# Kernel optimization log

Measured on AMD Instinct MI355X. Metric: run time of the kernel, lower is better.

## Reference

```python
import jax, jax.numpy as jnp
import numpy as np

NONLIN = jnp.tanh  # configurable gate/candidate nonlinearity ('nonlin' init arg)

T, B, I, H = 1024, 64, 256, 512


def setup_inputs() -> dict:
    key = jax.random.key(0)
    k1, k2, k3 = jax.random.split(key, 3)
    s_i = 1.0 / np.sqrt(I)
    s_h = 1.0 / np.sqrt(H)
    return {
        "x": jax.random.normal(k1, (T, B, I), dtype=jnp.float32),
        "Wi": jax.random.normal(k2, (I, 4 * H), dtype=jnp.float32) * s_i,
        "Wh": jax.random.normal(k3, (H, 4 * H), dtype=jnp.float32) * s_h,
        "bi": jnp.zeros((4 * H,), dtype=jnp.float32),
        "bh": jnp.zeros((4 * H,), dtype=jnp.float32),
        "h0": jnp.zeros((B, H), dtype=jnp.float32),
        "c0": jnp.zeros((B, H), dtype=jnp.float32),
    }


def reference(x, Wi, Wh, bi, bh, h0, c0):
    # Precompute input projection for all timesteps in one big GEMM: [T,B,4H]
    x_proj = jnp.einsum('tbi,ig->tbg', x, Wi) + bi

    def step(carry, xp_t):
        h, c = carry
        gates = xp_t + h @ Wh + bh            # [B, 4H]
        i_g, f_g, g_g, o_g = jnp.split(gates, 4, axis=-1)
        i_g = jax.nn.sigmoid(i_g)
        f_g = jax.nn.sigmoid(f_g)
        o_g = jax.nn.sigmoid(o_g)
        g_g = NONLIN(g_g)
        c_new = f_g * c + i_g * g_g
        h_new = o_g * NONLIN(c_new)
        return (h_new, c_new), h_new

    (h_T, c_T), hs = jax.lax.scan(step, (h0, c0), x_proj)
    return hs  # [T, B, H] hidden states for every timestep
```

## Files before the change

kernel.cpp:

```cpp
#include <hip/hip_runtime.h>
#include <math.h>


#define TT      1024
#define BB      64
#define II      256
#define HH      512
#define G4H     2048
#define RPB     16
#define NRG     4
#define NCG     64
#define THREADS 512

typedef short  bf16x8 __attribute__((ext_vector_type(8)));
typedef float  f32x4  __attribute__((ext_vector_type(4)));

__device__ __forceinline__ unsigned int cvtpk_bf16(float a, float b) {
    unsigned int r;
    asm volatile("v_cvt_pk_bf16_f32 %0, %1, %2" : "=v"(r) : "v"(a), "v"(b));
    return r;
}

__device__ __forceinline__ void coh_load4_f4(const float* p0, const float* p1,
                                             const float* p2, const float* p3,
                                             float4& a, float4& b,
                                             float4& c, float4& d) {
    asm volatile(
        "global_load_dwordx4 %0, %4, off sc0 sc1\n\t"
        "global_load_dwordx4 %1, %5, off sc0 sc1\n\t"
        "global_load_dwordx4 %2, %6, off sc0 sc1\n\t"
        "global_load_dwordx4 %3, %7, off sc0 sc1\n\t"
        "s_waitcnt vmcnt(0)"
        : "=&v"(a), "=&v"(b), "=&v"(c), "=&v"(d)
        : "v"(p0), "v"(p1), "v"(p2), "v"(p3)
        : "memory");
}
__device__ __forceinline__ void coh_store_f(float* p, float v) {
    asm volatile("global_store_dword %0, %1, off sc0 sc1"
                 :: "v"(p), "v"(v) : "memory");
}
__device__ __forceinline__ float fast_tanh(float v) {
    const float e = __expf(-2.0f * fabsf(v));
    const float r = (1.0f - e) / (1.0f + e);
    return v < 0.0f ? -r : r;
}
__device__ __forceinline__ float sigm(float v) {
    return 1.0f / (1.0f + __expf(-v));
}

__device__ __forceinline__ void stage_a(bf16x8* FH, bf16x8* FL,
                                        int kk, int r, int sub, float4 v) {
    const int lane_s = r + 16 * (sub >> 3);
    const int ui     = (sub & 7) >> 1;
    const unsigned int h0 = cvtpk_bf16(v.x, v.y);
    const unsigned int h1 = cvtpk_bf16(v.z, v.w);
    const float ax = __uint_as_float(h0 << 16);
    const float ay = __uint_as_float(h0 & 0xffff0000u);
    const float az = __uint_as_float(h1 << 16);
    const float aw = __uint_as_float(h1 & 0xffff0000u);
    const unsigned int l0 = cvtpk_bf16(v.x - ax, v.y - ay);
    const unsigned int l1 = cvtpk_bf16(v.z - az, v.w - aw);
    unsigned int* ph = (unsigned int*)&FH[kk * 64 + lane_s];
    unsigned int* pl = (unsigned int*)&FL[kk * 64 + lane_s];
    ph[ui] = h0; ph[ui + 1] = h1;
    pl[ui] = l0; pl[ui + 1] = l1;
}

__global__ void init_ctr(unsigned int* ctr) { ctr[threadIdx.x] = 0; }

__global__ __launch_bounds__(THREADS) void lstm_persist(
    const float* __restrict__ x,
    const float* __restrict__ Wi,
    const float* __restrict__ Wh,
    const float* __restrict__ bi,
    const float* __restrict__ bh,
    const float* __restrict__ h0p,
    const float* __restrict__ c0p,
    float* __restrict__ out,
    unsigned int* __restrict__ ctr)
{
    const int tid   = threadIdx.x;
    const int cg    = blockIdx.x & 63;
    const int rg    = blockIdx.x >> 6;
    const int row0  = rg * RPB;
    const int cell0 = cg * 8;
    const int wv    = tid >> 6;
    const int lane  = tid & 63;
    const int n2    = wv >> 2;
    const int k4    = wv & 3;

    __shared__ bf16x8 aFH[24 * 64];
    __shared__ bf16x8 aFL[24 * 64];
    __shared__ bf16x8 bFH[48 * 64];
    __shared__ bf16x8 bFL[48 * 64];
    __shared__ float  red[8 * 64 * 4];
    __shared__ float  c_lds[RPB][8];

    for (int i = 0; i < 24; ++i) {
        const int u     = tid + THREADS * i;
        const int upos  = u & 3;
        const int slice = u >> 2;
        const int lane_ = slice & 63;
        const int kk    = (slice >> 6) % 24;
        const int nn    = (slice >> 6) / 24;
        const int e0    = upos * 2;
        const int k     = kk * 32 + (lane_ >> 4) * 8 + e0;
        const int col   = nn * 16 + (lane_ & 15);
        const int J     = (col >> 3) * HH + cell0 + (col & 7);
        const float w0  = (k < II) ? Wi[(size_t)k * G4H + J]
                                   : Wh[(size_t)(k - II) * G4H + J];
        const float w1  = (k < II) ? Wi[(size_t)(k + 1) * G4H + J]
                                   : Wh[(size_t)(k + 1 - II) * G4H + J];
        const unsigned int hi = cvtpk_bf16(w0, w1);
        const float f0 = __uint_as_float(hi << 16);
        const float f1 = __uint_as_float(hi & 0xffff0000u);
        const unsigned int lo = cvtpk_bf16(w0 - f0, w1 - f1);
        ((unsigned int*)bFH)[u] = hi;
        ((unsigned int*)bFL)[u] = lo;
    }

    float b4[4];
    if (tid < 128) {
        const int r = tid >> 3, m8 = tid & 7;
        #pragma unroll
        for (int g = 0; g < 4; ++g)
            b4[g] = bi[g * HH + cell0 + m8] + bh[g * HH + cell0 + m8];
        c_lds[r][m8] = c0p[(size_t)(row0 + r) * HH + cell0 + m8];
    }

    #pragma unroll
    for (int i = 0; i < 2; ++i) {
        const int s = tid + THREADS * i, r = s >> 6, k = 4 * (s & 63);
        const float4 v = *(const float4*)(x + (size_t)(row0 + r) * II + k);
        stage_a(aFH, aFL, k >> 5, r, k & 31, v);
    }
    #pragma unroll
    for (int i = 0; i < 4; ++i) {
        const int s = tid + THREADS * i, r = s >> 7, k = 4 * (s & 127);
        const float4 v = *(const float4*)(h0p + (size_t)(row0 + r) * HH + k);
        stage_a(aFH, aFL, 8 + (k >> 5), r, k & 31, v);
    }
    __syncthreads();

    f32x4 acc = {0.f, 0.f, 0.f, 0.f};
    #pragma unroll
    for (int q = 0; q < 2; ++q) {
        const int kk = k4 * 2 + q;
        const bf16x8 ah = aFH[kk * 64 + lane];
        const bf16x8 al = aFL[kk * 64 + lane];
        const bf16x8 wh = bFH[(n2 * 24 + kk) * 64 + lane];
        const bf16x8 wl = bFL[(n2 * 24 + kk) * 64 + lane];
        acc = __builtin_amdgcn_mfma_f32_16x16x32_bf16(ah, wh, acc, 0, 0, 0);
        acc = __builtin_amdgcn_mfma_f32_16x16x32_bf16(ah, wl, acc, 0, 0, 0);
        acc = __builtin_amdgcn_mfma_f32_16x16x32_bf16(al, wh, acc, 0, 0, 0);
    }

    unsigned int* myctr = ctr + rg * 32;

    for (int t = 0; t < TT; ++t) {
        const bool more = (t + 1 < TT);

        float4 xr0, xr1;
        int xk0, xr0r, xk1, xr1r;
        if (more) {
            const int s0 = tid;       xr0r = s0 >> 6; xk0 = 4 * (s0 & 63);
            const int s1 = tid + 512; xr1r = s1 >> 6; xk1 = 4 * (s1 & 63);
            xr0 = *(const float4*)(x + ((size_t)(t + 1) * BB + row0 + xr0r) * II + xk0);
            xr1 = *(const float4*)(x + ((size_t)(t + 1) * BB + row0 + xr1r) * II + xk1);
        }

        #pragma unroll
        for (int q = 0; q < 4; ++q) {
            const int kk = 8 + k4 * 4 + q;
            const bf16x8 ah = aFH[kk * 64 + lane];
            const bf16x8 al = aFL[kk * 64 + lane];
            const bf16x8 wh = bFH[(n2 * 24 + kk) * 64 + lane];
            const bf16x8 wl = bFL[(n2 * 24 + kk) * 64 + lane];
            acc = __builtin_amdgcn_mfma_f32_16x16x32_bf16(ah, wh, acc, 0, 0, 0);
            acc = __builtin_amdgcn_mfma_f32_16x16x32_bf16(ah, wl, acc, 0, 0, 0);
            acc = __builtin_amdgcn_mfma_f32_16x16x32_bf16(al, wh, acc, 0, 0, 0);
        }

        ((f32x4*)red)[wv * 64 + lane] = acc;
        if (more) {
            stage_a(aFH, aFL, xk0 >> 5, xr0r, xk0 & 31, xr0);
            stage_a(aFH, aFL, xk1 >> 5, xr1r, xk1 & 31, xr1);
        }
        __syncthreads();

        if (tid < 128) {
            const int r = tid >> 3, m8 = tid & 7;
            const int lane_c_base = 16 * (r >> 2);
            const int reg = r & 3;
            float g4[4];
            #pragma unroll
            for (int g = 0; g < 4; ++g) {
                const int col = g * 8 + m8;
                const int nn  = col >> 4, cl = col & 15;
                const int lc  = cl + lane_c_base;
                float s = b4[g];
                #pragma unroll
                for (int p = 0; p < 4; ++p)
                    s += red[((nn * 4 + p) * 64 + lc) * 4 + reg];
                g4[g] = s;
            }
            const float ig = sigm(g4[0]);
            const float fg = sigm(g4[1]);
            const float gg = fast_tanh(g4[2]);
            const float og = sigm(g4[3]);
            const float cn = fg * c_lds[r][m8] + ig * gg;
            c_lds[r][m8] = cn;
            coh_store_f(out + ((size_t)t * BB + row0 + r) * HH + cell0 + m8,
                        og * fast_tanh(cn));
        }

        asm volatile("s_waitcnt vmcnt(0) lgkmcnt(0)" ::: "memory");
        __syncthreads();
        if (more) {
            if (tid == 0)
                __hip_atomic_fetch_add(myctr, 1u, __ATOMIC_RELAXED,
                                       __HIP_MEMORY_SCOPE_AGENT);

            acc = (f32x4){0.f, 0.f, 0.f, 0.f};
            #pragma unroll
            for (int q = 0; q < 2; ++q) {
                const int kk = k4 * 2 + q;
                const bf16x8 ah = aFH[kk * 64 + lane];
                const bf16x8 al = aFL[kk * 64 + lane];
                const bf16x8 wh = bFH[(n2 * 24 + kk) * 64 + lane];
                const bf16x8 wl = bFL[(n2 * 24 + kk) * 64 + lane];
                acc = __builtin_amdgcn_mfma_f32_16x16x32_bf16(ah, wh, acc, 0, 0, 0);
                acc = __builtin_amdgcn_mfma_f32_16x16x32_bf16(ah, wl, acc, 0, 0, 0);
                acc = __builtin_amdgcn_mfma_f32_16x16x32_bf16(al, wh, acc, 0, 0, 0);
            }

            if (tid == 0) {
                const unsigned int target = 64u * (unsigned int)(t + 1);
                while (__hip_atomic_load(myctr, __ATOMIC_RELAXED,
                                         __HIP_MEMORY_SCOPE_AGENT) < target) {
                    __builtin_amdgcn_s_sleep(2);
                }
            }
            __syncthreads();

            {
                const float* hb = out + (size_t)t * BB * HH;
                const int s0 = tid,        r0 = s0 >> 7, k0 = 4 * (s0 & 127);
                const int s1 = tid + 512,  r1 = s1 >> 7, k1 = 4 * (s1 & 127);
                const int s2 = tid + 1024, r2 = s2 >> 7, k2 = 4 * (s2 & 127);
                const int s3 = tid + 1536, r3 = s3 >> 7, k3 = 4 * (s3 & 127);
                float4 v0, v1, v2, v3;
                coh_load4_f4(hb + (size_t)(row0 + r0) * HH + k0,
                             hb + (size_t)(row0 + r1) * HH + k1,
                             hb + (size_t)(row0 + r2) * HH + k2,
                             hb + (size_t)(row0 + r3) * HH + k3,
                             v0, v1, v2, v3);
                stage_a(aFH, aFL, 8 + (k0 >> 5), r0, k0 & 31, v0);
                stage_a(aFH, aFL, 8 + (k1 >> 5), r1, k1 & 31, v1);
                stage_a(aFH, aFL, 8 + (k2 >> 5), r2, k2 & 31, v2);
                stage_a(aFH, aFL, 8 + (k3 >> 5), r3, k3 & 31, v3);
            }
            __syncthreads();
        }
    }
}

extern "C" void kernel_launch(void* const* d_in, const int* in_sizes, int n_in,
                              void* d_out, int out_size, void* d_ws, size_t ws_size,
                              hipStream_t stream) {
    const float* x  = (const float*)d_in[0];
    const float* Wi = (const float*)d_in[1];
    const float* Wh = (const float*)d_in[2];
    const float* bi = (const float*)d_in[3];
    const float* bh = (const float*)d_in[4];
    const float* h0 = (const float*)d_in[5];
    const float* c0 = (const float*)d_in[6];
    float* out = (float*)d_out;
    unsigned int* ctr = (unsigned int*)d_ws;

    init_ctr<<<1, 256, 0, stream>>>(ctr);

    void* args[] = { (void*)&x, (void*)&Wi, (void*)&Wh, (void*)&bi,
                     (void*)&bh, (void*)&h0, (void*)&c0, (void*)&out,
                     (void*)&ctr };
    hipError_t e = hipLaunchCooperativeKernel((const void*)lstm_persist,
                                              dim3(NRG * NCG), dim3(THREADS),
                                              args, 0, stream);
    if (e != hipSuccess) {
        (void)hipGetLastError();
        lstm_persist<<<dim3(NRG * NCG), dim3(THREADS), 0, stream>>>(
            x, Wi, Wh, bi, bh, h0, c0, out, ctr);
    }
}
```

Measured before the change: 4.524 ms.

## Keep weight fragments in registers and stage activation fragments with whole-vector LDS writes

Each wave now loads its six hi/lo bf16 weight fragments once into registers instead of storing all weights in shared memory and re-reading them every timestep. Activation staging is remapped so each thread converts eight contiguous floats and writes one full 16-byte fragment to LDS, replacing the scattered 32-bit stores. This cuts per-step LDS traffic and instruction count on the serial recurrence path. The cost is higher register pressure (24 extra VGPRs per lane for weights).

```diff
diff --git a/kernel.cpp b/kernel.cpp
--- a/kernel.cpp
+++ b/kernel.cpp
@@ -48,22 +48,20 @@
     return 1.0f / (1.0f + __expf(-v));
 }
 
-__device__ __forceinline__ void stage_a(bf16x8* FH, bf16x8* FL,
-                                        int kk, int r, int sub, float4 v) {
-    const int lane_s = r + 16 * (sub >> 3);
-    const int ui     = (sub & 7) >> 1;
-    const unsigned int h0 = cvtpk_bf16(v.x, v.y);
-    const unsigned int h1 = cvtpk_bf16(v.z, v.w);
-    const float ax = __uint_as_float(h0 << 16);
-    const float ay = __uint_as_float(h0 & 0xffff0000u);
-    const float az = __uint_as_float(h1 << 16);
-    const float aw = __uint_as_float(h1 & 0xffff0000u);
-    const unsigned int l0 = cvtpk_bf16(v.x - ax, v.y - ay);
-    const unsigned int l1 = cvtpk_bf16(v.z - az, v.w - aw);
-    unsigned int* ph = (unsigned int*)&FH[kk * 64 + lane_s];
-    unsigned int* pl = (unsigned int*)&FL[kk * 64 + lane_s];
-    ph[ui] = h0; ph[ui + 1] = h1;
-    pl[ui] = l0; pl[ui + 1] = l1;
+__device__ __forceinline__ void cvt_frag(float4 v0, float4 v1,
+                                         uint4& hi, uint4& lo) {
+    hi.x = cvtpk_bf16(v0.x, v0.y);
+    hi.y = cvtpk_bf16(v0.z, v0.w);
+    hi.z = cvtpk_bf16(v1.x, v1.y);
+    hi.w = cvtpk_bf16(v1.z, v1.w);
+    lo.x = cvtpk_bf16(v0.x - __uint_as_float(hi.x << 16),
+                      v0.y - __uint_as_float(hi.x & 0xffff0000u));
+    lo.y = cvtpk_bf16(v0.z - __uint_as_float(hi.y << 16),
+                      v0.w - __uint_as_float(hi.y & 0xffff0000u));
+    lo.z = cvtpk_bf16(v1.x - __uint_as_float(hi.z << 16),
+                      v1.y - __uint_as_float(hi.z & 0xffff0000u));
+    lo.w = cvtpk_bf16(v1.z - __uint_as_float(hi.w << 16),
+                      v1.w - __uint_as_float(hi.w & 0xffff0000u));
 }
 
 __global__ void init_ctr(unsigned int* ctr) { ctr[threadIdx.x] = 0; }
@@ -89,34 +87,36 @@
     const int n2    = wv >> 2;
     const int k4    = wv & 3;
 
-    __shared__ bf16x8 aFH[24 * 64];
-    __shared__ bf16x8 aFL[24 * 64];
-    __shared__ bf16x8 bFH[48 * 64];
-    __shared__ bf16x8 bFL[48 * 64];
-    __shared__ float  red[8 * 64 * 4];
-    __shared__ float  c_lds[RPB][8];
-
-    for (int i = 0; i < 24; ++i) {
-        const int u     = tid + THREADS * i;
-        const int upos  = u & 3;
-        const int slice = u >> 2;
-        const int lane_ = slice & 63;
-        const int kk    = (slice >> 6) % 24;
-        const int nn    = (slice >> 6) / 24;
-        const int e0    = upos * 2;
-        const int k     = kk * 32 + (lane_ >> 4) * 8 + e0;
-        const int col   = nn * 16 + (lane_ & 15);
-        const int J     = (col >> 3) * HH + cell0 + (col & 7);
-        const float w0  = (k < II) ? Wi[(size_t)k * G4H + J]
-                                   : Wh[(size_t)(k - II) * G4H + J];
-        const float w1  = (k < II) ? Wi[(size_t)(k + 1) * G4H + J]
-                                   : Wh[(size_t)(k + 1 - II) * G4H + J];
-        const unsigned int hi = cvtpk_bf16(w0, w1);
-        const float f0 = __uint_as_float(hi << 16);
-        const float f1 = __uint_as_float(hi & 0xffff0000u);
-        const unsigned int lo = cvtpk_bf16(w0 - f0, w1 - f1);
-        ((unsigned int*)bFH)[u] = hi;
-        ((unsigned int*)bFL)[u] = lo;
+    __shared__ uint4 aFH[24 * 64];
+    __shared__ uint4 aFL[24 * 64];
+    __shared__ float red[8 * 64 * 4];
+    __shared__ float c_lds[RPB][8];
+
+    const int s_ls = tid & 63;
+    const int s_r  = s_ls & 15;
+    const int s_kb = (tid >> 6) * 32 + ((s_ls >> 4) & 3) * 8;
+
+    bf16x8 wH[6], wL[6];
+    {
+        const int col = n2 * 16 + (lane & 15);
+        const int J   = (col >> 3) * HH + cell0 + (col & 7);
+        #pragma unroll
+        for (int s = 0; s < 6; ++s) {
+            const int kk = (s < 2) ? (k4 * 2 + s) : (8 + k4 * 4 + (s - 2));
+            const int kb = kk * 32 + (lane >> 4) * 8;
+            float w[8];
+            #pragma unroll
+            for (int e = 0; e < 8; ++e) {
+                const int k = kb + e;
+                w[e] = (k < II) ? Wi[(size_t)k * G4H + J]
+                                : Wh[(size_t)(k - II) * G4H + J];
+            }
+            uint4 hi, lo;
+            cvt_frag(make_float4(w[0], w[1], w[2], w[3]),
+                     make_float4(w[4], w[5], w[6], w[7]), hi, lo);
+            wH[s] = *(bf16x8*)&hi;
+            wL[s] = *(bf16x8*)&lo;
+        }
     }
 
     float b4[4];
@@ -128,17 +128,17 @@
         c_lds[r][m8] = c0p[(size_t)(row0 + r) * HH + cell0 + m8];
     }
 
-    #pragma unroll
-    for (int i = 0; i < 2; ++i) {
-        const int s = tid + THREADS * i, r = s >> 6, k = 4 * (s & 63);
-        const float4 v = *(const float4*)(x + (size_t)(row0 + r) * II + k);
-        stage_a(aFH, aFL, k >> 5, r, k & 31, v);
-    }
-    #pragma unroll
-    for (int i = 0; i < 4; ++i) {
-        const int s = tid + THREADS * i, r = s >> 7, k = 4 * (s & 127);
-        const float4 v = *(const float4*)(h0p + (size_t)(row0 + r) * HH + k);
-        stage_a(aFH, aFL, 8 + (k >> 5), r, k & 31, v);
+    {
+        const float* xr = x + (size_t)(row0 + s_r) * II + s_kb;
+        uint4 hi, lo;
+        cvt_frag(*(const float4*)xr, *(const float4*)(xr + 4), hi, lo);
+        aFH[tid] = hi; aFL[tid] = lo;
+
+        const float* hr = h0p + (size_t)(row0 + s_r) * HH + s_kb;
+        cvt_frag(*(const float4*)hr, *(const float4*)(hr + 4), hi, lo);
+        aFH[512 + tid] = hi; aFL[512 + tid] = lo;
+        cvt_frag(*(const float4*)(hr + 256), *(const float4*)(hr + 260), hi, lo);
+        aFH[1024 + tid] = hi; aFL[1024 + tid] = lo;
     }
     __syncthreads();
 
@@ -146,13 +146,11 @@
     #pragma unroll
     for (int q = 0; q < 2; ++q) {
         const int kk = k4 * 2 + q;
-        const bf16x8 ah = aFH[kk * 64 + lane];
-        const bf16x8 al = aFL[kk * 64 + lane];
-        const bf16x8 wh = bFH[(n2 * 24 + kk) * 64 + lane];
-        const bf16x8 wl = bFL[(n2 * 24 + kk) * 64 + lane];
-        acc = __builtin_amdgcn_mfma_f32_16x16x32_bf16(ah, wh, acc, 0, 0, 0);
-        acc = __builtin_amdgcn_mfma_f32_16x16x32_bf16(ah, wl, acc, 0, 0, 0);
-        acc = __builtin_amdgcn_mfma_f32_16x16x32_bf16(al, wh, acc, 0, 0, 0);
+        const bf16x8 ah = *(const bf16x8*)&aFH[kk * 64 + lane];
+        const bf16x8 al = *(const bf16x8*)&aFL[kk * 64 + lane];
+        acc = __builtin_amdgcn_mfma_f32_16x16x32_bf16(ah, wH[q], acc, 0, 0, 0);
+        acc = __builtin_amdgcn_mfma_f32_16x16x32_bf16(ah, wL[q], acc, 0, 0, 0);
+        acc = __builtin_amdgcn_mfma_f32_16x16x32_bf16(al, wH[q], acc, 0, 0, 0);
     }
 
     unsigned int* myctr = ctr + rg * 32;
@@ -160,31 +158,28 @@
     for (int t = 0; t < TT; ++t) {
         const bool more = (t + 1 < TT);
 
-        float4 xr0, xr1;
-        int xk0, xr0r, xk1, xr1r;
+        float4 xv0, xv1;
         if (more) {
-            const int s0 = tid;       xr0r = s0 >> 6; xk0 = 4 * (s0 & 63);
-            const int s1 = tid + 512; xr1r = s1 >> 6; xk1 = 4 * (s1 & 63);
-            xr0 = *(const float4*)(x + ((size_t)(t + 1) * BB + row0 + xr0r) * II + xk0);
-            xr1 = *(const float4*)(x + ((size_t)(t + 1) * BB + row0 + xr1r) * II + xk1);
+            const float* xr = x + ((size_t)(t + 1) * BB + row0 + s_r) * II + s_kb;
+            xv0 = *(const float4*)xr;
+            xv1 = *(const float4*)(xr + 4);
         }
 
         #pragma unroll
         for (int q = 0; q < 4; ++q) {
             const int kk = 8 + k4 * 4 + q;
-            const bf16x8 ah = aFH[kk * 64 + lane];
-            const bf16x8 al = aFL[kk * 64 + lane];
-            const bf16x8 wh = bFH[(n2 * 24 + kk) * 64 + lane];
-            const bf16x8 wl = bFL[(n2 * 24 + kk) * 64 + lane];
-            acc = __builtin_amdgcn_mfma_f32_16x16x32_bf16(ah, wh, acc, 0, 0, 0);
-            acc = __builtin_amdgcn_mfma_f32_16x16x32_bf16(ah, wl, acc, 0, 0, 0);
-            acc = __builtin_amdgcn_mfma_f32_16x16x32_bf16(al, wh, acc, 0, 0, 0);
+            const bf16x8 ah = *(const bf16x8*)&aFH[kk * 64 + lane];
+            const bf16x8 al = *(const bf16x8*)&aFL[kk * 64 + lane];
+            acc = __builtin_amdgcn_mfma_f32_16x16x32_bf16(ah, wH[2 + q], acc, 0, 0, 0);
+            acc = __builtin_amdgcn_mfma_f32_16x16x32_bf16(ah, wL[2 + q], acc, 0, 0, 0);
+            acc = __builtin_amdgcn_mfma_f32_16x16x32_bf16(al, wH[2 + q], acc, 0, 0, 0);
         }
 
         ((f32x4*)red)[wv * 64 + lane] = acc;
         if (more) {
-            stage_a(aFH, aFL, xk0 >> 5, xr0r, xk0 & 31, xr0);
-            stage_a(aFH, aFL, xk1 >> 5, xr1r, xk1 & 31, xr1);
+            uint4 hi, lo;
+            cvt_frag(xv0, xv1, hi, lo);
+            aFH[tid] = hi; aFL[tid] = lo;
         }
         __syncthreads();
 
@@ -225,13 +220,11 @@
             #pragma unroll
             for (int q = 0; q < 2; ++q) {
                 const int kk = k4 * 2 + q;
-                const bf16x8 ah = aFH[kk * 64 + lane];
-                const bf16x8 al = aFL[kk * 64 + lane];
-                const bf16x8 wh = bFH[(n2 * 24 + kk) * 64 + lane];
-                const bf16x8 wl = bFL[(n2 * 24 + kk) * 64 + lane];
-                acc = __builtin_amdgcn_mfma_f32_16x16x32_bf16(ah, wh, acc, 0, 0, 0);
-                acc = __builtin_amdgcn_mfma_f32_16x16x32_bf16(ah, wl, acc, 0, 0, 0);
-                acc = __builtin_amdgcn_mfma_f32_16x16x32_bf16(al, wh, acc, 0, 0, 0);
+                const bf16x8 ah = *(const bf16x8*)&aFH[kk * 64 + lane];
+                const bf16x8 al = *(const bf16x8*)&aFL[kk * 64 + lane];
+                acc = __builtin_amdgcn_mfma_f32_16x16x32_bf16(ah, wH[q], acc, 0, 0, 0);
+                acc = __builtin_amdgcn_mfma_f32_16x16x32_bf16(ah, wL[q], acc, 0, 0, 0);
+                acc = __builtin_amdgcn_mfma_f32_16x16x32_bf16(al, wH[q], acc, 0, 0, 0);
             }
 
             if (tid == 0) {
@@ -244,21 +237,15 @@
             __syncthreads();
 
             {
-                const float* hb = out + (size_t)t * BB * HH;
-                const int s0 = tid,        r0 = s0 >> 7, k0 = 4 * (s0 & 127);
-                const int s1 = tid + 512,  r1 = s1 >> 7, k1 = 4 * (s1 & 127);
-                const int s2 = tid + 1024, r2 = s2 >> 7, k2 = 4 * (s2 & 127);
-                const int s3 = tid + 1536, r3 = s3 >> 7, k3 = 4 * (s3 & 127);
+                const float* hr = out + (size_t)t * BB * HH
+                                  + (size_t)(row0 + s_r) * HH + s_kb;
                 float4 v0, v1, v2, v3;
-                coh_load4_f4(hb + (size_t)(row0 + r0) * HH + k0,
-                             hb + (size_t)(row0 + r1) * HH + k1,
-                             hb + (size_t)(row0 + r2) * HH + k2,
-                             hb + (size_t)(row0 + r3) * HH + k3,
-                             v0, v1, v2, v3);
-                stage_a(aFH, aFL, 8 + (k0 >> 5), r0, k0 & 31, v0);
-                stage_a(aFH, aFL, 8 + (k1 >> 5), r1, k1 & 31, v1);
-                stage_a(aFH, aFL, 8 + (k2 >> 5), r2, k2 & 31, v2);
-                stage_a(aFH, aFL, 8 + (k3 >> 5), r3, k3 & 31, v3);
+                coh_load4_f4(hr, hr + 4, hr + 256, hr + 260, v0, v1, v2, v3);
+                uint4 hi, lo;
+                cvt_frag(v0, v1, hi, lo);
+                aFH[512 + tid] = hi; aFL[512 + tid] = lo;
+                cvt_frag(v2, v3, hi, lo);
+                aFH[1024 + tid] = hi; aFL[1024 + tid] = lo;
             }
             __syncthreads();
         }
```

After: 4.105 ms. 1.1x faster.
